# Optimization experiments

Measured on AMD Instinct MI355X. Metric: run time of the kernel, lower is better.

## Reference

```python
import jax, jax.numpy as jnp
import numpy as np

B, D, R, E = 16384, 512, 64, 8

def setup_inputs() -> dict:
    key = jax.random.key(0)
    ks = jax.random.split(key, 8)
    return {
        "x0": jax.random.normal(ks[0], (B, D), jnp.float32),
        "x": jax.random.normal(ks[1], (B, D), jnp.float32),
        "U": jax.random.normal(ks[2], (E, D, R), jnp.float32) * 0.02,
        "V": jax.random.normal(ks[3], (E, R, D), jnp.float32) * 0.02,
        "C": jax.random.normal(ks[4], (E, R, R), jnp.float32) * 0.02,
        "b": jnp.zeros((E, D), jnp.float32),
        "Wg": jax.random.normal(ks[5], (E, D), jnp.float32) * 0.02,
        "bg": jnp.zeros((E,), jnp.float32),
    }

def reference(x0, x, U, V, C, b, Wg, bg):
    # gate: softmax over experts
    g = jax.nn.softmax(x @ Wg.T + bg, axis=1)            # [B, E]
    # per-expert low-rank bilinear transform, batched over experts
    xv = jnp.einsum('bd,erd->ber', x, V)                 # x @ V[e].T
    xvc = jnp.einsum('ber,ers->bes', xv, C)              # xv @ C[e]
    proj = jnp.einsum('bes,eds->bed', xvc, U)            # xvc @ U[e].T
    # gated sum: sum_e g_e * (x0*proj_e + b_e + x)
    gproj = jnp.einsum('be,bed->bd', g, proj)
    out = x0 * gproj + g @ b + x * g.sum(axis=1, keepdims=True)
    return out
```

## Files before the change

kernel.cpp:

```cpp
#include <hip/hip_runtime.h>
#include <math.h>


typedef __bf16 bf16_t;
typedef __attribute__((ext_vector_type(8))) __bf16 bf16x8;
typedef __attribute__((ext_vector_type(4))) __bf16 bf16x4;
typedef __attribute__((ext_vector_type(4))) float  floatx4;

__device__ __forceinline__ void async16(void* lds, const void* gp) {
  __builtin_amdgcn_global_load_lds(
      (__attribute__((address_space(1))) void*)(gp),
      (__attribute__((address_space(3))) void*)(lds), 16, 0, 0);
}

__global__ __launch_bounds__(256) void prep_kernel(
    const float* __restrict__ U, const float* __restrict__ V, const float* __restrict__ C,
    bf16_t* __restrict__ VCc, bf16_t* __restrict__ Ut) {
  int tid = blockIdx.x * 256 + threadIdx.x;
  if (tid < 512 * 512) {
    int n = tid >> 9, d = tid & 511;
    int e = n >> 6, s = n & 63;
    const float* Vp = V + (size_t)e * 64 * 512 + d;
    const float* Cp = C + (size_t)e * 64 * 64 + s;
    float acc = 0.f;
#pragma unroll 8
    for (int r = 0; r < 64; ++r) acc += Vp[(size_t)r * 512] * Cp[r * 64];
    VCc[tid] = (bf16_t)acc;
  } else {
    int i2 = tid - 512 * 512;
    int d = i2 >> 9, n = i2 & 511;
    int e = n >> 6, s = n & 63;
    Ut[i2] = (bf16_t)U[((size_t)e * 512 + d) * 64 + s];
  }
}

__global__ __launch_bounds__(256) void gate_kernel(
    const float* __restrict__ x, const float* __restrict__ Wg, const float* __restrict__ bg,
    bf16_t* __restrict__ xbf, float* __restrict__ g) {
  int wave = threadIdx.x >> 6, lane = threadIdx.x & 63;
  int row = blockIdx.x * 4 + wave;
  const float4* xr = (const float4*)(x + (size_t)row * 512);
  float4 v0 = xr[lane];
  float4 v1 = xr[lane + 64];
  bf16x4* xb = (bf16x4*)(xbf + (size_t)row * 512);
  bf16x4 b0, b1;
  b0.x = (bf16_t)v0.x; b0.y = (bf16_t)v0.y; b0.z = (bf16_t)v0.z; b0.w = (bf16_t)v0.w;
  b1.x = (bf16_t)v1.x; b1.y = (bf16_t)v1.y; b1.z = (bf16_t)v1.z; b1.w = (bf16_t)v1.w;
  xb[lane] = b0;
  xb[lane + 64] = b1;
  float acc[8];
#pragma unroll
  for (int e = 0; e < 8; ++e) {
    const float4* wp = (const float4*)(Wg + (size_t)e * 512);
    float4 w0 = wp[lane], w1 = wp[lane + 64];
    acc[e] = v0.x * w0.x + v0.y * w0.y + v0.z * w0.z + v0.w * w0.w +
             v1.x * w1.x + v1.y * w1.y + v1.z * w1.z + v1.w * w1.w;
  }
#pragma unroll
  for (int e = 0; e < 8; ++e) {
#pragma unroll
    for (int off = 32; off > 0; off >>= 1) acc[e] += __shfl_xor(acc[e], off, 64);
  }
  float z[8], mx = -1e30f;
#pragma unroll
  for (int e = 0; e < 8; ++e) { z[e] = acc[e] + bg[e]; mx = fmaxf(mx, z[e]); }
  float s = 0.f;
#pragma unroll
  for (int e = 0; e < 8; ++e) { z[e] = __expf(z[e] - mx); s += z[e]; }
  float inv = 1.f / s;
  if (lane == 0) {
#pragma unroll
    for (int e = 0; e < 8; ++e) g[(size_t)row * 8 + e] = z[e] * inv;
  }
}

__device__ __forceinline__ void gemm_core64(
    const bf16_t* __restrict__ A, const bf16_t* __restrict__ Bt,
    int m0, int n0, int t, floatx4 acc[4][2]) {
  __shared__ char lds[24576];
  char* ldsA = lds;
  char* ldsB = lds + 16384;
  const int wave = t >> 6, lane = t & 63;
  const int wr = wave >> 1, wc = wave & 1;
  const int lhi = lane >> 4, llo = lane & 15;
#pragma unroll 1
  for (int it = 0; it < 8; ++it) {
    const int k0 = it * 64;
    __syncthreads();
#pragma unroll
    for (int i = 0; i < 4; ++i) {
      int c = i * 256 + t;
      int r = c >> 3, q = c & 7;
      int p = q ^ (r & 7);
      async16(ldsA + (i * 256 + wave * 64) * 16,
              (const char*)A + (size_t)(m0 + r) * 1024 + k0 * 2 + p * 16);
    }
#pragma unroll
    for (int i = 0; i < 2; ++i) {
      int c = i * 256 + t;
      int r = c >> 3, q = c & 7;
      int p = q ^ (r & 7);
      async16(ldsB + (i * 256 + wave * 64) * 16,
              (const char*)Bt + (size_t)(n0 + r) * 1024 + k0 * 2 + p * 16);
    }
    __syncthreads();
#pragma unroll
    for (int ks = 0; ks < 2; ++ks) {
      bf16x8 af[4], bfm[2];
#pragma unroll
      for (int i = 0; i < 4; ++i) {
        int rA = wr * 64 + i * 16 + llo;
        af[i] = *(const bf16x8*)(ldsA + rA * 128 + (((ks * 4 + lhi) ^ (rA & 7)) << 4));
      }
#pragma unroll
      for (int j = 0; j < 2; ++j) {
        int rB = wc * 32 + j * 16 + llo;
        bfm[j] = *(const bf16x8*)(ldsB + rB * 128 + (((ks * 4 + lhi) ^ (rB & 7)) << 4));
      }
#pragma unroll
      for (int i = 0; i < 4; ++i)
#pragma unroll
        for (int j = 0; j < 2; ++j)
          acc[i][j] = __builtin_amdgcn_mfma_f32_16x16x32_bf16(af[i], bfm[j], acc[i][j], 0, 0, 0);
    }
  }
}

__global__ __launch_bounds__(256, 4) void gemm1_kernel(
    const bf16_t* __restrict__ xbf, const bf16_t* __restrict__ VCc,
    const float* __restrict__ g, bf16_t* __restrict__ T) {
  int t = threadIdx.x;
  int m0 = blockIdx.x * 128, n0 = blockIdx.y * 64;
  floatx4 acc[4][2];
#pragma unroll
  for (int i = 0; i < 4; ++i)
#pragma unroll
    for (int j = 0; j < 2; ++j) acc[i][j] = (floatx4){0.f, 0.f, 0.f, 0.f};
  gemm_core64(xbf, VCc, m0, n0, t, acc);
  const int wave = t >> 6, lane = t & 63;
  const int wr = wave >> 1, wc = wave & 1;
  const int lhi = lane >> 4, llo = lane & 15;
  const int e = n0 >> 6;
#pragma unroll
  for (int i = 0; i < 4; ++i) {
#pragma unroll
    for (int r = 0; r < 4; ++r) {
      int m = m0 + wr * 64 + i * 16 + lhi * 4 + r;
      float gv = g[(size_t)m * 8 + e];
#pragma unroll
      for (int j = 0; j < 2; ++j) {
        int n = n0 + wc * 32 + j * 16 + llo;
        T[(size_t)m * 512 + n] = (bf16_t)(acc[i][j][r] * gv);
      }
    }
  }
}

__global__ __launch_bounds__(256, 4) void gemm2_kernel(
    const bf16_t* __restrict__ T, const bf16_t* __restrict__ Ut,
    const float* __restrict__ g, const float* __restrict__ bvec,
    const float* __restrict__ x0, const float* __restrict__ x,
    float* __restrict__ out) {
  int t = threadIdx.x;
  int m0 = blockIdx.x * 128, n0 = blockIdx.y * 64;
  floatx4 acc[4][2];
#pragma unroll
  for (int i = 0; i < 4; ++i)
#pragma unroll
    for (int j = 0; j < 2; ++j) acc[i][j] = (floatx4){0.f, 0.f, 0.f, 0.f};
  gemm_core64(T, Ut, m0, n0, t, acc);
  const int wave = t >> 6, lane = t & 63;
  const int wr = wave >> 1, wc = wave & 1;
  const int lhi = lane >> 4, llo = lane & 15;
  float bb[2][8];
#pragma unroll
  for (int j = 0; j < 2; ++j) {
    int n = n0 + wc * 32 + j * 16 + llo;
#pragma unroll
    for (int e = 0; e < 8; ++e) bb[j][e] = bvec[(size_t)e * 512 + n];
  }
#pragma unroll
  for (int i = 0; i < 4; ++i) {
#pragma unroll
    for (int r = 0; r < 4; ++r) {
      int m = m0 + wr * 64 + i * 16 + lhi * 4 + r;
      float g8[8], gsum = 0.f;
#pragma unroll
      for (int e = 0; e < 8; ++e) { g8[e] = g[(size_t)m * 8 + e]; gsum += g8[e]; }
#pragma unroll
      for (int j = 0; j < 2; ++j) {
        int n = n0 + wc * 32 + j * 16 + llo;
        float bias = 0.f;
#pragma unroll
        for (int e = 0; e < 8; ++e) bias += g8[e] * bb[j][e];
        size_t idx = (size_t)m * 512 + n;
        out[idx] = x0[idx] * acc[i][j][r] + bias + x[idx] * gsum;
      }
    }
  }
}

extern "C" void kernel_launch(void* const* d_in, const int* in_sizes, int n_in,
                              void* d_out, int out_size, void* d_ws, size_t ws_size,
                              hipStream_t stream) {
  const float* x0 = (const float*)d_in[0];
  const float* x  = (const float*)d_in[1];
  const float* U  = (const float*)d_in[2];
  const float* V  = (const float*)d_in[3];
  const float* C  = (const float*)d_in[4];
  const float* bv = (const float*)d_in[5];
  const float* Wg = (const float*)d_in[6];
  const float* bg = (const float*)d_in[7];
  float* out = (float*)d_out;

  char* ws = (char*)d_ws;
  bf16_t* xbf = (bf16_t*)(ws);
  bf16_t* T   = (bf16_t*)(ws + 16777216);
  bf16_t* VCc = (bf16_t*)(ws + 33554432);
  bf16_t* Ut  = (bf16_t*)(ws + 34078720);
  float*  g   = (float*)(ws + 34603008);

  prep_kernel<<<2048, 256, 0, stream>>>(U, V, C, VCc, Ut);
  gate_kernel<<<4096, 256, 0, stream>>>(x, Wg, bg, xbf, g);
  gemm1_kernel<<<dim3(128, 8), 256, 0, stream>>>(xbf, VCc, g, T);
  gemm2_kernel<<<dim3(128, 8), 256, 0, stream>>>(T, Ut, g, bv, x0, x, out);
}
```

Baseline: 163.2 us.

## Replace async LDS loads with register-staged prefetch pipeline in GEMM core

The GEMM main loop now loads the next K-tile from global memory into registers while the current tile is being computed from LDS, then writes it to LDS. This replaces the previous global_load_lds path, which used a load/sync/compute pattern with no overlap. The epilogues also stage gate values and bias rows in LDS, replacing scattered per-thread global reads. The cost is extra registers for the staged tiles, more barriers per iteration, and a redundant prefetch on the final iteration.

```diff
diff --git a/kernel.cpp b/kernel.cpp
--- a/kernel.cpp
+++ b/kernel.cpp
@@ -6,12 +6,6 @@
 typedef __attribute__((ext_vector_type(8))) __bf16 bf16x8;
 typedef __attribute__((ext_vector_type(4))) __bf16 bf16x4;
 typedef __attribute__((ext_vector_type(4))) float  floatx4;
-
-__device__ __forceinline__ void async16(void* lds, const void* gp) {
-  __builtin_amdgcn_global_load_lds(
-      (__attribute__((address_space(1))) void*)(gp),
-      (__attribute__((address_space(3))) void*)(lds), 16, 0, 0);
-}
 
 __global__ __launch_bounds__(256) void prep_kernel(
     const float* __restrict__ U, const float* __restrict__ V, const float* __restrict__ C,
@@ -74,61 +68,75 @@
   }
 }
 
-__device__ __forceinline__ void gemm_core64(
-    const bf16_t* __restrict__ A, const bf16_t* __restrict__ Bt,
-    int m0, int n0, int t, floatx4 acc[4][2]) {
-  __shared__ char lds[24576];
-  char* ldsA = lds;
-  char* ldsB = lds + 16384;
-  const int wave = t >> 6, lane = t & 63;
-  const int wr = wave >> 1, wc = wave & 1;
+struct StageRegs { float4 a[4]; float4 b[2]; };
+
+__device__ __forceinline__ void load_tile(const char* gA, const char* gB, int it, StageRegs& s) {
+#pragma unroll
+  for (int i = 0; i < 4; ++i)
+    s.a[i] = *(const float4*)(gA + it * 128 + (size_t)i * 32 * 1024);
+#pragma unroll
+  for (int j = 0; j < 2; ++j)
+    s.b[j] = *(const float4*)(gB + it * 128 + (size_t)j * 32 * 1024);
+}
+
+__device__ __forceinline__ void write_tile(char* wA, char* wB, const StageRegs& s) {
+#pragma unroll
+  for (int i = 0; i < 4; ++i) *(float4*)(wA + i * 32 * 128) = s.a[i];
+#pragma unroll
+  for (int j = 0; j < 2; ++j) *(float4*)(wB + j * 32 * 128) = s.b[j];
+}
+
+__device__ __forceinline__ void compute_tile(const char* ldsA, const char* ldsB,
+                                             int wr, int wc, int lhi, int llo,
+                                             floatx4 acc[4][2]) {
+#pragma unroll
+  for (int ks = 0; ks < 2; ++ks) {
+    const int sw = (((ks * 4 + lhi) ^ (llo & 7)) << 4);
+    bf16x8 bfm[2];
+#pragma unroll
+    for (int j = 0; j < 2; ++j)
+      bfm[j] = *(const bf16x8*)(ldsB + (wc * 32 + j * 16 + llo) * 128 + sw);
+#pragma unroll
+    for (int i = 0; i < 4; ++i) {
+      bf16x8 af = *(const bf16x8*)(ldsA + (wr * 64 + i * 16 + llo) * 128 + sw);
+      acc[i][0] = __builtin_amdgcn_mfma_f32_16x16x32_bf16(af, bfm[0], acc[i][0], 0, 0, 0);
+      acc[i][1] = __builtin_amdgcn_mfma_f32_16x16x32_bf16(af, bfm[1], acc[i][1], 0, 0, 0);
+    }
+  }
+}
+
+__device__ __forceinline__ void gemm_pipe(const bf16_t* A, const bf16_t* Bt,
+                                          int m0, int n0, int t,
+                                          char* ldsA, char* ldsB, floatx4 acc[4][2]) {
+  const int lane = t & 63;
+  const int wr = t >> 7, wc = (t >> 6) & 1;
   const int lhi = lane >> 4, llo = lane & 15;
+  const int rs = t >> 3, qs = t & 7;
+  const char* gA = (const char*)A + (size_t)(m0 + rs) * 1024 + qs * 16;
+  const char* gB = (const char*)Bt + (size_t)(n0 + rs) * 1024 + qs * 16;
+  char* wA = ldsA + rs * 128 + ((qs ^ (rs & 7)) << 4);
+  char* wB = ldsB + rs * 128 + ((qs ^ (rs & 7)) << 4);
+  StageRegs r0, r1;
+  load_tile(gA, gB, 0, r0);
 #pragma unroll 1
-  for (int it = 0; it < 8; ++it) {
-    const int k0 = it * 64;
-    __syncthreads();
-#pragma unroll
-    for (int i = 0; i < 4; ++i) {
-      int c = i * 256 + t;
-      int r = c >> 3, q = c & 7;
-      int p = q ^ (r & 7);
-      async16(ldsA + (i * 256 + wave * 64) * 16,
-              (const char*)A + (size_t)(m0 + r) * 1024 + k0 * 2 + p * 16);
-    }
-#pragma unroll
-    for (int i = 0; i < 2; ++i) {
-      int c = i * 256 + t;
-      int r = c >> 3, q = c & 7;
-      int p = q ^ (r & 7);
-      async16(ldsB + (i * 256 + wave * 64) * 16,
-              (const char*)Bt + (size_t)(n0 + r) * 1024 + k0 * 2 + p * 16);
-    }
-    __syncthreads();
-#pragma unroll
-    for (int ks = 0; ks < 2; ++ks) {
-      bf16x8 af[4], bfm[2];
-#pragma unroll
-      for (int i = 0; i < 4; ++i) {
-        int rA = wr * 64 + i * 16 + llo;
-        af[i] = *(const bf16x8*)(ldsA + rA * 128 + (((ks * 4 + lhi) ^ (rA & 7)) << 4));
-      }
-#pragma unroll
-      for (int j = 0; j < 2; ++j) {
-        int rB = wc * 32 + j * 16 + llo;
-        bfm[j] = *(const bf16x8*)(ldsB + rB * 128 + (((ks * 4 + lhi) ^ (rB & 7)) << 4));
-      }
-#pragma unroll
-      for (int i = 0; i < 4; ++i)
-#pragma unroll
-        for (int j = 0; j < 2; ++j)
-          acc[i][j] = __builtin_amdgcn_mfma_f32_16x16x32_bf16(af[i], bfm[j], acc[i][j], 0, 0, 0);
-    }
+  for (int it = 0; it < 8; it += 2) {
+    write_tile(wA, wB, r0);
+    __syncthreads();
+    load_tile(gA, gB, it + 1, r1);
+    compute_tile(ldsA, ldsB, wr, wc, lhi, llo, acc);
+    __syncthreads();
+    write_tile(wA, wB, r1);
+    __syncthreads();
+    load_tile(gA, gB, (it + 2 < 8) ? it + 2 : 0, r0);
+    compute_tile(ldsA, ldsB, wr, wc, lhi, llo, acc);
+    __syncthreads();
   }
 }
 
 __global__ __launch_bounds__(256, 4) void gemm1_kernel(
     const bf16_t* __restrict__ xbf, const bf16_t* __restrict__ VCc,
     const float* __restrict__ g, bf16_t* __restrict__ T) {
+  __shared__ char lds[24576];
   int t = threadIdx.x;
   int m0 = blockIdx.x * 128, n0 = blockIdx.y * 64;
   floatx4 acc[4][2];
@@ -136,17 +144,21 @@
   for (int i = 0; i < 4; ++i)
 #pragma unroll
     for (int j = 0; j < 2; ++j) acc[i][j] = (floatx4){0.f, 0.f, 0.f, 0.f};
-  gemm_core64(xbf, VCc, m0, n0, t, acc);
-  const int wave = t >> 6, lane = t & 63;
-  const int wr = wave >> 1, wc = wave & 1;
+  gemm_pipe(xbf, VCc, m0, n0, t, lds, lds + 16384, acc);
+  float* ldsG = (float*)lds;
+  const int e = n0 >> 6;
+  if (t < 128) ldsG[t] = g[(size_t)(m0 + t) * 8 + e];
+  __syncthreads();
+  const int lane = t & 63;
+  const int wr = t >> 7, wc = (t >> 6) & 1;
   const int lhi = lane >> 4, llo = lane & 15;
-  const int e = n0 >> 6;
 #pragma unroll
   for (int i = 0; i < 4; ++i) {
 #pragma unroll
     for (int r = 0; r < 4; ++r) {
-      int m = m0 + wr * 64 + i * 16 + lhi * 4 + r;
-      float gv = g[(size_t)m * 8 + e];
+      int rml = wr * 64 + i * 16 + lhi * 4 + r;
+      float gv = ldsG[rml];
+      int m = m0 + rml;
 #pragma unroll
       for (int j = 0; j < 2; ++j) {
         int n = n0 + wc * 32 + j * 16 + llo;
@@ -161,6 +173,7 @@
     const float* __restrict__ g, const float* __restrict__ bvec,
     const float* __restrict__ x0, const float* __restrict__ x,
     float* __restrict__ out) {
+  __shared__ char lds[24576];
   int t = threadIdx.x;
   int m0 = blockIdx.x * 128, n0 = blockIdx.y * 64;
   floatx4 acc[4][2];
@@ -168,25 +181,33 @@
   for (int i = 0; i < 4; ++i)
 #pragma unroll
     for (int j = 0; j < 2; ++j) acc[i][j] = (floatx4){0.f, 0.f, 0.f, 0.f};
-  gemm_core64(T, Ut, m0, n0, t, acc);
-  const int wave = t >> 6, lane = t & 63;
-  const int wr = wave >> 1, wc = wave & 1;
+  gemm_pipe(T, Ut, m0, n0, t, lds, lds + 16384, acc);
+  float* ldsG = (float*)lds;
+  float* ldsBv = (float*)(lds + 4096);
+  ((float4*)ldsG)[t] = ((const float4*)(g + (size_t)m0 * 8))[t];
+  if (t < 128)
+    ((float4*)ldsBv)[t] = ((const float4*)bvec)[(t >> 4) * 128 + (n0 >> 2) + (t & 15)];
+  __syncthreads();
+  const int lane = t & 63;
+  const int wr = t >> 7, wc = (t >> 6) & 1;
   const int lhi = lane >> 4, llo = lane & 15;
   float bb[2][8];
 #pragma unroll
   for (int j = 0; j < 2; ++j) {
-    int n = n0 + wc * 32 + j * 16 + llo;
-#pragma unroll
-    for (int e = 0; e < 8; ++e) bb[j][e] = bvec[(size_t)e * 512 + n];
+    int nl = wc * 32 + j * 16 + llo;
+#pragma unroll
+    for (int e = 0; e < 8; ++e) bb[j][e] = ldsBv[e * 64 + nl];
   }
 #pragma unroll
   for (int i = 0; i < 4; ++i) {
 #pragma unroll
     for (int r = 0; r < 4; ++r) {
-      int m = m0 + wr * 64 + i * 16 + lhi * 4 + r;
-      float g8[8], gsum = 0.f;
-#pragma unroll
-      for (int e = 0; e < 8; ++e) { g8[e] = g[(size_t)m * 8 + e]; gsum += g8[e]; }
+      int rml = wr * 64 + i * 16 + lhi * 4 + r;
+      float4 ga = ((const float4*)ldsG)[rml * 2];
+      float4 gb2 = ((const float4*)ldsG)[rml * 2 + 1];
+      float g8[8] = {ga.x, ga.y, ga.z, ga.w, gb2.x, gb2.y, gb2.z, gb2.w};
+      float gsum = g8[0] + g8[1] + g8[2] + g8[3] + g8[4] + g8[5] + g8[6] + g8[7];
+      int m = m0 + rml;
 #pragma unroll
       for (int j = 0; j < 2; ++j) {
         int n = n0 + wc * 32 + j * 16 + llo;
```

Measured after the change: 290.7 us. 1.78x slower.
